# Kernel tuning notes

Measured on AMD Instinct MI355X. Metric: run time of the kernel, lower is better.

Reference implementation:

```python
import jax, jax.numpy as jnp
import numpy as np

H = 1024        # hidden_size
I = 512         # moe_intermediate_size
E = 16          # n_routed_experts
K = 2           # num_experts_per_tok
N_SHARED = 2    # n_shared_experts
IS = I * N_SHARED  # shared expert intermediate
B, S = 2, 2048


def setup_inputs() -> dict:
    key = jax.random.key(0)
    ks = jax.random.split(key, 9)
    sc = 0.02
    return {
        "hidden_states": jax.random.normal(ks[0], (B, S, H), jnp.float32),
        "router_w":     jax.random.normal(ks[1], (E, H), jnp.float32) * sc,
        "expert_gate":  jax.random.normal(ks[2], (E, H, I), jnp.float32) * sc,
        "expert_up":    jax.random.normal(ks[3], (E, H, I), jnp.float32) * sc,
        "expert_down":  jax.random.normal(ks[4], (E, I, H), jnp.float32) * sc,
        "shared_gate":  jax.random.normal(ks[5], (H, IS), jnp.float32) * sc,
        "shared_up":    jax.random.normal(ks[6], (H, IS), jnp.float32) * sc,
        "shared_down":  jax.random.normal(ks[7], (IS, H), jnp.float32) * sc,
    }


def reference(hidden_states, router_w, expert_gate, expert_up, expert_down,
              shared_gate, shared_up, shared_down):
    orig_shape = hidden_states.shape
    x = hidden_states.reshape(-1, H)            # [T, H]
    T = x.shape[0]

    # --- MoEGate: softmax router scores, top-k, normalized weights ---
    scores = jax.nn.softmax(x @ router_w.T, axis=-1)        # [T, E]
    topk_w, topk_idx = jax.lax.top_k(scores, K)             # [T, K]
    topk_w = topk_w / jnp.sum(topk_w, axis=-1, keepdims=True)  # norm_topk_prob

    # Sparse combine weights as dense [T, E] gate matrix (scatter of top-k).
    gates = jnp.zeros((T, E), x.dtype).at[jnp.arange(T)[:, None], topk_idx].add(topk_w)

    # --- Routed experts: gated SiLU MLP per expert, weighted combine ---
    g = jnp.einsum('th,ehi->tei', x, expert_gate)           # [T, E, I]
    u = jnp.einsum('th,ehi->tei', x, expert_up)             # [T, E, I]
    a = jax.nn.silu(g) * u                                  # [T, E, I]
    y = jnp.einsum('tei,eih,te->th', a, expert_down, gates) # [T, H]

    # --- Shared experts ---
    s = (jax.nn.silu(x @ shared_gate) * (x @ shared_up)) @ shared_down  # [T, H]

    return (y + s).reshape(orig_shape)
```

## Files before the change

kernel.cpp:

```cpp
#include <hip/hip_runtime.h>
#include <math.h>

#define H_DIM 1024
#define I_DIM 512
#define E_NUM 16
#define T_TOK 4096
#define IS_DIM 1024
#define CSTR 32

#define P_RT   1024
#define P_WU   (P_RT + 2048)
#define P_SG   (P_WU + 2048)
#define P_SU   (P_SG + 256)
#define P_END  (P_SU + 256)

#define G_GEMM 1152
#define G_TR   2304
#define G_END  (G_GEMM + G_TR)

#define D_GRID 896

typedef unsigned short u16;
typedef __attribute__((ext_vector_type(8))) short short8;
typedef __attribute__((ext_vector_type(4))) float floatx4;

__device__ __forceinline__ float bf2f(u16 u) {
    union { unsigned int u; float f; } c; c.u = ((unsigned int)u) << 16; return c.f;
}
__device__ __forceinline__ u16 f2bf(float f) {
    union { float f; unsigned int u; } c; c.f = f;
    unsigned int r = (c.u + 0x7fffu + ((c.u >> 16) & 1u)) >> 16;
    return (u16)r;
}
__device__ __forceinline__ void gld16(const u16* g, u16* l) {
    __builtin_amdgcn_global_load_lds(
        (const __attribute__((address_space(1))) unsigned int*)g,
        (__attribute__((address_space(3))) unsigned int*)l, 16, 0, 0);
}

__device__ __forceinline__ void tr64(const float* src, u16* dst, int R, int C,
                                     int local, u16* tile)
{
    int tpm = (R >> 6) * (C >> 6);
    int mat = local / tpm;
    int tl_ = local - mat * tpm;
    int tcn = C >> 6;
    int tr = tl_ / tcn, tc = tl_ - tr * tcn;
    src += (size_t)mat * R * C;
    dst += (size_t)mat * R * C;
    int t = threadIdx.x;
    int r0 = t >> 2, c0 = (t & 3) << 4;
    const float* sp = src + (size_t)(tr * 64 + r0) * C + tc * 64 + c0;
    #pragma unroll
    for (int j = 0; j < 16; j += 4) {
        float4 v = *(const float4*)(sp + j);
        tile[r0 * 65 + c0 + j + 0] = f2bf(v.x);
        tile[r0 * 65 + c0 + j + 1] = f2bf(v.y);
        tile[r0 * 65 + c0 + j + 2] = f2bf(v.z);
        tile[r0 * 65 + c0 + j + 3] = f2bf(v.w);
    }
    __syncthreads();
    int cW = t >> 2, rW = (t & 3) << 4;
    u16 tmp[16];
    #pragma unroll
    for (int j = 0; j < 16; ++j) tmp[j] = tile[(rW + j) * 65 + cW];
    u16* dp = dst + (size_t)(tc * 64 + cW) * R + tr * 64 + rW;
    *(uint4*)(dp)     = *(const uint4*)(tmp);
    *(uint4*)(dp + 8) = *(const uint4*)(tmp + 8);
}

__device__ __forceinline__ int derive_routed(int gi, const int* cnt,
                                             int& e, int& mt, int& sub, int& abase)
{
    int off = 0, b = 0;
    #pragma unroll
    for (int ee = 0; ee < E_NUM; ++ee) {
        int mts = (cnt[ee * CSTR] + 127) >> 7;
        int span = mts << 3;
        if (gi < off + span) {
            int local = gi - off;
            e = ee; mt = local >> 3; sub = local & 7; abase = b;
            return 1;
        }
        off += span; b += mts << 7;
    }
    return 0;
}

__global__ __launch_bounds__(256, 4)
void k_prep(const float* x, const float* rw,
            const float* wg, const float* wu, const float* sg, const float* su,
            u16* wgt, u16* wut, u16* sgt, u16* sut,
            u16* xb, float* topkw, int* elist, int* cnt)
{
    __shared__ u16 tile[64 * 65];
    int bi = blockIdx.x;
    if (bi >= P_RT) {
        if (bi < P_WU)      tr64(wg, wgt, 1024, 512,  bi - P_RT, tile);
        else if (bi < P_SG) tr64(wu, wut, 1024, 512,  bi - P_WU, tile);
        else if (bi < P_SU) tr64(sg, sgt, 1024, 1024, bi - P_SG, tile);
        else                tr64(su, sut, 1024, 1024, bi - P_SU, tile);
        return;
    }
    int lane = threadIdx.x & 63;
    int wv = threadIdx.x >> 6;
    int t = bi * 4 + wv;
    const float* xr = x + (size_t)t * H_DIM;
    float xv[16];
    #pragma unroll
    for (int j = 0; j < 16; ++j) xv[j] = xr[j * 64 + lane];
    u16* xrow = xb + (size_t)t * H_DIM;
    #pragma unroll
    for (int j = 0; j < 16; ++j) xrow[j * 64 + lane] = f2bf(xv[j]);
    float sc[E_NUM];
    #pragma unroll
    for (int e = 0; e < E_NUM; ++e) sc[e] = 0.f;
    #pragma unroll
    for (int e = 0; e < E_NUM; ++e) {
        const float* rr = rw + e * H_DIM;
        #pragma unroll
        for (int j = 0; j < 16; ++j) sc[e] += xv[j] * rr[j * 64 + lane];
    }
    #pragma unroll
    for (int off = 32; off > 0; off >>= 1) {
        float tmp[E_NUM];
        #pragma unroll
        for (int e = 0; e < E_NUM; ++e) tmp[e] = __shfl_xor(sc[e], off, 64);
        #pragma unroll
        for (int e = 0; e < E_NUM; ++e) sc[e] += tmp[e];
    }
    if (lane == 0) {
        float b1 = -1e30f, b2 = -1e30f; int i1 = 0, i2 = 0;
        #pragma unroll
        for (int e = 0; e < E_NUM; ++e) {
            if (sc[e] > b1) { b2 = b1; i2 = i1; b1 = sc[e]; i1 = e; }
            else if (sc[e] > b2) { b2 = sc[e]; i2 = e; }
        }
        float w1 = 1.f / (1.f + __expf(b2 - b1));
        float w2 = 1.f - w1;
        topkw[t * 2]     = w1;
        topkw[t * 2 + 1] = w2;
        int p1 = atomicAdd(&cnt[i1 * CSTR], 1); elist[i1 * T_TOK + p1] = (t << 1);
        int p2 = atomicAdd(&cnt[i2 * CSTR], 1); elist[i2 * T_TOK + p2] = (t << 1) | 1;
    }
}

__global__ __launch_bounds__(256, 3)
void k_gateup(const u16* xb, const u16* wgt, const u16* wut,
              const u16* sgt, const u16* sut,
              const float* wd, const float* sd, u16* wdt, u16* sdt,
              const int* elist, const int* cnt,
              u16* act, u16* sact)
{
    __shared__ u16 smem[128 * 64 + 64 * 64 + 64 * 64];
    int bi = blockIdx.x;
    if (bi >= G_GEMM) {
        int tb = bi - G_GEMM;
        if (tb < 2048) tr64(wd, wdt, 512, 1024, tb, smem);
        else           tr64(sd, sdt, 1024, 1024, tb - 2048, smem);
        return;
    }
    int kind, e = 0, mt, cb, abase = 0;
    if (bi < 512) { kind = 1; mt = bi >> 4; cb = bi & 15; }
    else {
        kind = 0;
        if (!derive_routed(bi - 512, cnt, e, mt, cb, abase)) return;
    }

    u16* lA = smem;
    u16* lG = smem + 8192;
    u16* lU = smem + 12288;
    int tid = threadIdx.x, lane = tid & 63, w = tid >> 6;
    int srow = lane >> 2, scp = lane & 3;

    const u16* gb = kind ? sgt : (wgt + (size_t)e * I_DIM * H_DIM);
    const u16* ub = kind ? sut : (wut + (size_t)e * I_DIM * H_DIM);
    int c = cnt[e * CSTR];

    const u16 *gA[2], *gG, *gU;
    u16 *dA[2], *dG, *dU;
    #pragma unroll
    for (int jj = 0; jj < 2; ++jj) {
        int call = w * 2 + jj;
        int row = call * 16 + srow;
        int gc = scp ^ ((row >> 1) & 3);
        int tok;
        if (kind) tok = mt * 128 + row;
        else {
            int p = mt * 128 + row;
            int pc = p < c ? p : c - 1;
            tok = elist[e * T_TOK + pc] >> 1;
        }
        gA[jj] = xb + (size_t)tok * H_DIM + gc * 8;
        dA[jj] = lA + call * 512;
    }
    {
        int row = w * 16 + srow;
        int gc = scp ^ ((row >> 1) & 3);
        gG = gb + (size_t)(cb * 64 + row) * H_DIM + gc * 8;
        gU = ub + (size_t)(cb * 64 + row) * H_DIM + gc * 8;
        dG = lG + w * 512;
        dU = lU + w * 512;
    }

    int wr = w >> 1, wc = w & 1;
    int quad = lane >> 4, l15 = lane & 15;
    const u16 *fA[4], *fG[2], *fU[2];
    #pragma unroll
    for (int i = 0; i < 4; ++i) {
        int r = wr * 64 + i * 16 + l15;
        fA[i] = lA + r * 32 + (quad ^ ((r >> 1) & 3)) * 8;
    }
    #pragma unroll
    for (int j = 0; j < 2; ++j) {
        int n = wc * 32 + j * 16 + l15;
        fG[j] = lG + n * 32 + (quad ^ ((n >> 1) & 3)) * 8;
        fU[j] = lU + n * 32 + (quad ^ ((n >> 1) & 3)) * 8;
    }

    floatx4 accg[4][2], accu[4][2];
    #pragma unroll
    for (int i = 0; i < 4; ++i)
        #pragma unroll
        for (int j = 0; j < 2; ++j)
            #pragma unroll
            for (int r = 0; r < 4; ++r) { accg[i][j][r] = 0.f; accu[i][j][r] = 0.f; }

    for (int s = 0; s < H_DIM / 64; ++s) {
        #pragma unroll
        for (int q = 0; q < 2; ++q) {
            gld16(gA[0] + q * 32, dA[0] + q * 4096);
            gld16(gA[1] + q * 32, dA[1] + q * 4096);
            gld16(gG + q * 32, dG + q * 2048);
            gld16(gU + q * 32, dU + q * 2048);
        }
        gA[0] += 64; gA[1] += 64; gG += 64; gU += 64;
        __syncthreads();
        #pragma unroll
        for (int q = 0; q < 2; ++q) {
            short8 a[4], g[2], u[2];
            #pragma unroll
            for (int i = 0; i < 4; ++i) a[i] = *(const short8*)(fA[i] + q * 4096);
            #pragma unroll
            for (int j = 0; j < 2; ++j) {
                g[j] = *(const short8*)(fG[j] + q * 2048);
                u[j] = *(const short8*)(fU[j] + q * 2048);
            }
            #pragma unroll
            for (int i = 0; i < 4; ++i)
                #pragma unroll
                for (int j = 0; j < 2; ++j) {
                    accg[i][j] = __builtin_amdgcn_mfma_f32_16x16x32_bf16(a[i], g[j], accg[i][j], 0, 0, 0);
                    accu[i][j] = __builtin_amdgcn_mfma_f32_16x16x32_bf16(a[i], u[j], accu[i][j], 0, 0, 0);
                }
        }
        __syncthreads();
    }

    u16* obase = kind ? (sact + (size_t)(mt * 128) * IS_DIM)
                      : (act + (size_t)(abase + mt * 128) * I_DIM);
    int old = kind ? IS_DIM : I_DIM;
    #pragma unroll
    for (int i = 0; i < 4; ++i)
        #pragma unroll
        for (int j = 0; j < 2; ++j)
            #pragma unroll
            for (int r = 0; r < 4; ++r) {
                int row = wr * 64 + i * 16 + quad * 4 + r;
                int col = cb * 64 + wc * 32 + j * 16 + l15;
                float gg = accg[i][j][r], uu = accu[i][j][r];
                float aa = gg / (1.f + __expf(-gg)) * uu;
                obase[(size_t)row * old + col] = f2bf(aa);
            }
}

__global__ __launch_bounds__(256, 3)
void k_down(const u16* act, const u16* sact, const u16* wdt, const u16* sdt,
            const int* elist, const int* cnt, const float* topkw,
            u16* y0, u16* y1, float* out)
{
    int bi = blockIdx.x;
    int kind, e = 0, mt, nb, abase = 0;
    if (bi < 256) { kind = 1; mt = bi >> 3; nb = bi & 7; }
    else {
        kind = 0;
        if (!derive_routed(bi - 256, cnt, e, mt, nb, abase)) return;
    }

    __shared__ u16 smem[128 * 64 * 2];
    u16* lA = smem;
    u16* lB = smem + 8192;
    int tid = threadIdx.x, lane = tid & 63, w = tid >> 6;
    int srow = lane >> 2, scp = lane & 3;

    int K = kind ? IS_DIM : I_DIM;
    const u16* ab = kind ? (sact + (size_t)(mt * 128) * IS_DIM)
                         : (act + (size_t)(abase + mt * 128) * I_DIM);
    const u16* bb = kind ? (sdt + (size_t)(nb * 128) * IS_DIM)
                         : (wdt + ((size_t)e * H_DIM + nb * 128) * I_DIM);
    int c = cnt[e * CSTR];

    const u16 *gA[2], *gB[2];
    u16 *dA[2], *dB[2];
    #pragma unroll
    for (int jj = 0; jj < 2; ++jj) {
        int call = w * 2 + jj;
        int row = call * 16 + srow;
        int gc = scp ^ ((row >> 1) & 3);
        gA[jj] = ab + (size_t)row * K + gc * 8;
        dA[jj] = lA + call * 512;
        gB[jj] = bb + (size_t)row * K + gc * 8;
        dB[jj] = lB + call * 512;
    }

    int wr = w >> 1, wc = w & 1;
    int quad = lane >> 4, l15 = lane & 15;
    const u16 *fA[4], *fB[4];
    #pragma unroll
    for (int i = 0; i < 4; ++i) {
        int r = wr * 64 + i * 16 + l15;
        fA[i] = lA + r * 32 + (quad ^ ((r >> 1) & 3)) * 8;
    }
    #pragma unroll
    for (int j = 0; j < 4; ++j) {
        int n = wc * 64 + j * 16 + l15;
        fB[j] = lB + n * 32 + (quad ^ ((n >> 1) & 3)) * 8;
    }

    floatx4 acc[4][4];
    #pragma unroll
    for (int i = 0; i < 4; ++i)
        #pragma unroll
        for (int j = 0; j < 4; ++j)
            #pragma unroll
            for (int r = 0; r < 4; ++r) acc[i][j][r] = 0.f;

    int steps = K >> 6;
    for (int s = 0; s < steps; ++s) {
        #pragma unroll
        for (int q = 0; q < 2; ++q) {
            gld16(gA[0] + q * 32, dA[0] + q * 4096);
            gld16(gA[1] + q * 32, dA[1] + q * 4096);
            gld16(gB[0] + q * 32, dB[0] + q * 4096);
            gld16(gB[1] + q * 32, dB[1] + q * 4096);
        }
        gA[0] += 64; gA[1] += 64; gB[0] += 64; gB[1] += 64;
        __syncthreads();
        #pragma unroll
        for (int q = 0; q < 2; ++q) {
            short8 a[4], b[4];
            #pragma unroll
            for (int i = 0; i < 4; ++i) a[i] = *(const short8*)(fA[i] + q * 4096);
            #pragma unroll
            for (int j = 0; j < 4; ++j) b[j] = *(const short8*)(fB[j] + q * 4096);
            #pragma unroll
            for (int i = 0; i < 4; ++i)
                #pragma unroll
                for (int j = 0; j < 4; ++j)
                    acc[i][j] = __builtin_amdgcn_mfma_f32_16x16x32_bf16(a[i], b[j], acc[i][j], 0, 0, 0);
        }
        __syncthreads();
    }

    if (kind) {
        #pragma unroll
        for (int i = 0; i < 4; ++i)
            #pragma unroll
            for (int j = 0; j < 4; ++j)
                #pragma unroll
                for (int r = 0; r < 4; ++r) {
                    int row = mt * 128 + wr * 64 + i * 16 + quad * 4 + r;
                    int col = nb * 128 + wc * 64 + j * 16 + l15;
                    out[(size_t)row * H_DIM + col] = acc[i][j][r];
                }
    } else {
        #pragma unroll
        for (int i = 0; i < 4; ++i)
            #pragma unroll
            for (int r = 0; r < 4; ++r) {
                int row = wr * 64 + i * 16 + quad * 4 + r;
                int p = mt * 128 + row;
                if (p < c) {
                    int ent = elist[e * T_TOK + p];
                    int t = ent >> 1, sl = ent & 1;
                    float wt = topkw[t * 2 + sl];
                    u16* yb = sl ? y1 : y0;
                    #pragma unroll
                    for (int j = 0; j < 4; ++j) {
                        int col = nb * 128 + wc * 64 + j * 16 + l15;
                        yb[(size_t)t * H_DIM + col] = f2bf(wt * acc[i][j][r]);
                    }
                }
            }
    }
}

__global__ __launch_bounds__(256)
void k_final(float* out, const u16* y0, const u16* y1)
{
    int i = blockIdx.x * 256 + threadIdx.x;
    float4 o = ((const float4*)out)[i];
    uint2 a = ((const uint2*)y0)[i];
    uint2 b = ((const uint2*)y1)[i];
    const u16* pa = (const u16*)&a;
    const u16* pb = (const u16*)&b;
    o.x += bf2f(pa[0]) + bf2f(pb[0]);
    o.y += bf2f(pa[1]) + bf2f(pb[1]);
    o.z += bf2f(pa[2]) + bf2f(pb[2]);
    o.w += bf2f(pa[3]) + bf2f(pb[3]);
    ((float4*)out)[i] = o;
}

extern "C" void kernel_launch(void* const* d_in, const int* in_sizes, int n_in,
                              void* d_out, int out_size, void* d_ws, size_t ws_size,
                              hipStream_t stream)
{
    const float* x  = (const float*)d_in[0];
    const float* rw = (const float*)d_in[1];
    const float* wg = (const float*)d_in[2];
    const float* wu = (const float*)d_in[3];
    const float* wd = (const float*)d_in[4];
    const float* sg = (const float*)d_in[5];
    const float* su = (const float*)d_in[6];
    const float* sd = (const float*)d_in[7];
    float* out = (float*)d_out;

    char* ws = (char*)d_ws;
    const size_t MB = 1024ull * 1024ull;
    u16* wgt  = (u16*)(ws);
    u16* wut  = (u16*)(ws + 16 * MB);
    u16* wdt  = (u16*)(ws + 32 * MB);
    u16* sgt  = (u16*)(ws + 48 * MB);
    u16* sut  = (u16*)(ws + 50 * MB);
    u16* sdt  = (u16*)(ws + 52 * MB);
    u16* xb   = (u16*)(ws + 54 * MB);
    u16* act  = (u16*)(ws + 62 * MB);
    u16* sact = (u16*)(ws + 72 * MB);
    u16* y0   = (u16*)(ws + 80 * MB);
    u16* y1   = (u16*)(ws + 88 * MB);
    float* topkw  = (float*)(ws + 96 * MB);
    int* elist    = (int*)(ws + 96 * MB + 64 * 1024);
    int* cnt      = (int*)(ws + 97 * MB);

    hipMemsetAsync(cnt, 0, E_NUM * CSTR * sizeof(int), stream);
    k_prep<<<P_END, 256, 0, stream>>>(x, rw, wg, wu, sg, su,
                                      wgt, wut, sgt, sut,
                                      xb, topkw, elist, cnt);
    k_gateup<<<G_END, 256, 0, stream>>>(xb, wgt, wut, sgt, sut,
                                        wd, sd, wdt, sdt,
                                        elist, cnt, act, sact);
    k_down<<<D_GRID, 256, 0, stream>>>(act, sact, wdt, sdt,
                                       elist, cnt, topkw, y0, y1, out);
    k_final<<<T_TOK * H_DIM / 4 / 256, 256, 0, stream>>>(out, y0, y1);
}
```

Baseline: 271.1 us.

## Enlarge gate/up and down GEMM tiles and add block index swizzle

Doubles the N-tile of the gate/up GEMM from 64 to 128 columns and of the down GEMM from 128 to 256 columns, halving the grid sizes and the number of routed sub-tiles per expert. Each block now reuses every loaded A tile across more weight columns, cutting redundant reads of activations and the per-block fixed overhead. Block indices are also permuted across groups of 8 to change how neighbouring blocks are scheduled. The larger accumulator arrays raise register and LDS use, and occupancy hints drop from 3 to 2 blocks per CU, which could reduce latency hiding and leave fewer blocks to fill the machine. The workspace offsets are also shifted.

```diff
diff --git a/kernel.cpp b/kernel.cpp
--- a/kernel.cpp
+++ b/kernel.cpp
@@ -14,11 +14,11 @@
 #define P_SU   (P_SG + 256)
 #define P_END  (P_SU + 256)
 
-#define G_GEMM 1152
+#define G_GEMM 576
 #define G_TR   2304
 #define G_END  (G_GEMM + G_TR)
 
-#define D_GRID 896
+#define D_GRID 448
 
 typedef unsigned short u16;
 typedef __attribute__((ext_vector_type(8))) short short8;
@@ -76,10 +76,10 @@
     #pragma unroll
     for (int ee = 0; ee < E_NUM; ++ee) {
         int mts = (cnt[ee * CSTR] + 127) >> 7;
-        int span = mts << 3;
+        int span = mts << 2;
         if (gi < off + span) {
             int local = gi - off;
-            e = ee; mt = local >> 3; sub = local & 7; abase = b;
+            e = ee; mt = local >> 2; sub = local & 3; abase = b;
             return 1;
         }
         off += span; b += mts << 7;
@@ -145,14 +145,14 @@
     }
 }
 
-__global__ __launch_bounds__(256, 3)
+__global__ __launch_bounds__(256, 2)
 void k_gateup(const u16* xb, const u16* wgt, const u16* wut,
               const u16* sgt, const u16* sut,
               const float* wd, const float* sd, u16* wdt, u16* sdt,
               const int* elist, const int* cnt,
               u16* act, u16* sact)
 {
-    __shared__ u16 smem[128 * 64 + 64 * 64 + 64 * 64];
+    __shared__ u16 smem[24576];
     int bi = blockIdx.x;
     if (bi >= G_GEMM) {
         int tb = bi - G_GEMM;
@@ -160,16 +160,14 @@
         else           tr64(sd, sdt, 1024, 1024, tb - 2048, smem);
         return;
     }
+    bi = (bi & 7) * (G_GEMM / 8) + (bi >> 3);
     int kind, e = 0, mt, cb, abase = 0;
-    if (bi < 512) { kind = 1; mt = bi >> 4; cb = bi & 15; }
+    if (bi < 256) { kind = 1; mt = bi >> 3; cb = bi & 7; }
     else {
         kind = 0;
-        if (!derive_routed(bi - 512, cnt, e, mt, cb, abase)) return;
-    }
-
-    u16* lA = smem;
-    u16* lG = smem + 8192;
-    u16* lU = smem + 12288;
+        if (!derive_routed(bi - 256, cnt, e, mt, cb, abase)) return;
+    }
+
     int tid = threadIdx.x, lane = tid & 63, w = tid >> 6;
     int srow = lane >> 2, scp = lane & 3;
 
@@ -177,12 +175,11 @@
     const u16* ub = kind ? sut : (wut + (size_t)e * I_DIM * H_DIM);
     int c = cnt[e * CSTR];
 
-    const u16 *gA[2], *gG, *gU;
-    u16 *dA[2], *dG, *dU;
-    #pragma unroll
-    for (int jj = 0; jj < 2; ++jj) {
-        int call = w * 2 + jj;
-        int row = call * 16 + srow;
+    const u16 *pA[2], *pG[2], *pU[2];
+    int dA[2], dB[2];
+    #pragma unroll
+    for (int i = 0; i < 2; ++i) {
+        int row = w * 32 + i * 16 + srow;
         int gc = scp ^ ((row >> 1) & 3);
         int tok;
         if (kind) tok = mt * 128 + row;
@@ -191,65 +188,64 @@
             int pc = p < c ? p : c - 1;
             tok = elist[e * T_TOK + pc] >> 1;
         }
-        gA[jj] = xb + (size_t)tok * H_DIM + gc * 8;
-        dA[jj] = lA + call * 512;
-    }
-    {
-        int row = w * 16 + srow;
-        int gc = scp ^ ((row >> 1) & 3);
-        gG = gb + (size_t)(cb * 64 + row) * H_DIM + gc * 8;
-        gU = ub + (size_t)(cb * 64 + row) * H_DIM + gc * 8;
-        dG = lG + w * 512;
-        dU = lU + w * 512;
+        pA[i] = xb + (size_t)tok * H_DIM + gc * 8;
+        dA[i] = w * 1024 + i * 512;
+        int n = cb * 128 + row;
+        pG[i] = gb + (size_t)n * H_DIM + gc * 8;
+        pU[i] = ub + (size_t)n * H_DIM + gc * 8;
+        dB[i] = w * 1024 + i * 512;
     }
 
     int wr = w >> 1, wc = w & 1;
     int quad = lane >> 4, l15 = lane & 15;
-    const u16 *fA[4], *fG[2], *fU[2];
+    int fA[4], fB[4];
     #pragma unroll
     for (int i = 0; i < 4; ++i) {
         int r = wr * 64 + i * 16 + l15;
-        fA[i] = lA + r * 32 + (quad ^ ((r >> 1) & 3)) * 8;
-    }
-    #pragma unroll
-    for (int j = 0; j < 2; ++j) {
-        int n = wc * 32 + j * 16 + l15;
-        fG[j] = lG + n * 32 + (quad ^ ((n >> 1) & 3)) * 8;
-        fU[j] = lU + n * 32 + (quad ^ ((n >> 1) & 3)) * 8;
-    }
-
-    floatx4 accg[4][2], accu[4][2];
+        fA[i] = r * 32 + (quad ^ ((r >> 1) & 3)) * 8;
+    }
+    #pragma unroll
+    for (int j = 0; j < 4; ++j) {
+        int n = wc * 64 + j * 16 + l15;
+        fB[j] = n * 32 + (quad ^ ((n >> 1) & 3)) * 8;
+    }
+
+    floatx4 accg[4][4], accu[4][4];
     #pragma unroll
     for (int i = 0; i < 4; ++i)
         #pragma unroll
-        for (int j = 0; j < 2; ++j)
+        for (int j = 0; j < 4; ++j)
             #pragma unroll
             for (int r = 0; r < 4; ++r) { accg[i][j][r] = 0.f; accu[i][j][r] = 0.f; }
 
     for (int s = 0; s < H_DIM / 64; ++s) {
         #pragma unroll
         for (int q = 0; q < 2; ++q) {
-            gld16(gA[0] + q * 32, dA[0] + q * 4096);
-            gld16(gA[1] + q * 32, dA[1] + q * 4096);
-            gld16(gG + q * 32, dG + q * 2048);
-            gld16(gU + q * 32, dU + q * 2048);
-        }
-        gA[0] += 64; gA[1] += 64; gG += 64; gU += 64;
+            int k = s * 64 + q * 32;
+            u16* c0 = smem + q * 4096;
+            gld16(pA[0] + k, c0 + dA[0]);
+            gld16(pA[1] + k, c0 + dA[1]);
+            gld16(pG[0] + k, c0 + 8192 + dB[0]);
+            gld16(pG[1] + k, c0 + 8192 + dB[1]);
+            gld16(pU[0] + k, c0 + 16384 + dB[0]);
+            gld16(pU[1] + k, c0 + 16384 + dB[1]);
+        }
         __syncthreads();
         #pragma unroll
         for (int q = 0; q < 2; ++q) {
-            short8 a[4], g[2], u[2];
-            #pragma unroll
-            for (int i = 0; i < 4; ++i) a[i] = *(const short8*)(fA[i] + q * 4096);
-            #pragma unroll
-            for (int j = 0; j < 2; ++j) {
-                g[j] = *(const short8*)(fG[j] + q * 2048);
-                u[j] = *(const short8*)(fU[j] + q * 2048);
+            const u16* cb_ = smem + q * 4096;
+            short8 a[4], g[4], u[4];
+            #pragma unroll
+            for (int i = 0; i < 4; ++i) a[i] = *(const short8*)(cb_ + fA[i]);
+            #pragma unroll
+            for (int j = 0; j < 4; ++j) {
+                g[j] = *(const short8*)(cb_ + 8192 + fB[j]);
+                u[j] = *(const short8*)(cb_ + 16384 + fB[j]);
             }
             #pragma unroll
             for (int i = 0; i < 4; ++i)
                 #pragma unroll
-                for (int j = 0; j < 2; ++j) {
+                for (int j = 0; j < 4; ++j) {
                     accg[i][j] = __builtin_amdgcn_mfma_f32_16x16x32_bf16(a[i], g[j], accg[i][j], 0, 0, 0);
                     accu[i][j] = __builtin_amdgcn_mfma_f32_16x16x32_bf16(a[i], u[j], accu[i][j], 0, 0, 0);
                 }
@@ -263,75 +259,78 @@
     #pragma unroll
     for (int i = 0; i < 4; ++i)
         #pragma unroll
-        for (int j = 0; j < 2; ++j)
+        for (int j = 0; j < 4; ++j)
             #pragma unroll
             for (int r = 0; r < 4; ++r) {
                 int row = wr * 64 + i * 16 + quad * 4 + r;
-                int col = cb * 64 + wc * 32 + j * 16 + l15;
+                int col = cb * 128 + wc * 64 + j * 16 + l15;
                 float gg = accg[i][j][r], uu = accu[i][j][r];
                 float aa = gg / (1.f + __expf(-gg)) * uu;
                 obase[(size_t)row * old + col] = f2bf(aa);
             }
 }
 
-__global__ __launch_bounds__(256, 3)
+__global__ __launch_bounds__(256, 2)
 void k_down(const u16* act, const u16* sact, const u16* wdt, const u16* sdt,
             const int* elist, const int* cnt, const float* topkw,
             u16* y0, u16* y1, float* out)
 {
     int bi = blockIdx.x;
+    bi = (bi & 7) * (D_GRID / 8) + (bi >> 3);
     int kind, e = 0, mt, nb, abase = 0;
-    if (bi < 256) { kind = 1; mt = bi >> 3; nb = bi & 7; }
+    if (bi < 128) { kind = 1; mt = bi >> 2; nb = bi & 3; }
     else {
         kind = 0;
-        if (!derive_routed(bi - 256, cnt, e, mt, nb, abase)) return;
-    }
-
-    __shared__ u16 smem[128 * 64 * 2];
-    u16* lA = smem;
-    u16* lB = smem + 8192;
+        if (!derive_routed(bi - 128, cnt, e, mt, nb, abase)) return;
+    }
+
+    __shared__ u16 smem[24576];
     int tid = threadIdx.x, lane = tid & 63, w = tid >> 6;
     int srow = lane >> 2, scp = lane & 3;
 
     int K = kind ? IS_DIM : I_DIM;
     const u16* ab = kind ? (sact + (size_t)(mt * 128) * IS_DIM)
                          : (act + (size_t)(abase + mt * 128) * I_DIM);
-    const u16* bb = kind ? (sdt + (size_t)(nb * 128) * IS_DIM)
-                         : (wdt + ((size_t)e * H_DIM + nb * 128) * I_DIM);
+    const u16* bb = kind ? sdt : (wdt + (size_t)e * H_DIM * I_DIM);
     int c = cnt[e * CSTR];
 
-    const u16 *gA[2], *gB[2];
-    u16 *dA[2], *dB[2];
-    #pragma unroll
-    for (int jj = 0; jj < 2; ++jj) {
-        int call = w * 2 + jj;
-        int row = call * 16 + srow;
+    const u16 *pA[2], *pB[4];
+    int dA[2], dB[4];
+    #pragma unroll
+    for (int i = 0; i < 2; ++i) {
+        int row = w * 32 + i * 16 + srow;
         int gc = scp ^ ((row >> 1) & 3);
-        gA[jj] = ab + (size_t)row * K + gc * 8;
-        dA[jj] = lA + call * 512;
-        gB[jj] = bb + (size_t)row * K + gc * 8;
-        dB[jj] = lB + call * 512;
+        pA[i] = ab + (size_t)row * K + gc * 8;
+        dA[i] = w * 1024 + i * 512;
+    }
+    #pragma unroll
+    for (int i = 0; i < 4; ++i) {
+        int ln = w * 64 + i * 16 + srow;
+        int n = nb * 256 + ln;
+        int gc = scp ^ ((ln >> 1) & 3);
+        pB[i] = bb + (size_t)n * K + gc * 8;
+        dB[i] = w * 2048 + i * 512;
     }
 
     int wr = w >> 1, wc = w & 1;
     int quad = lane >> 4, l15 = lane & 15;
-    const u16 *fA[4], *fB[4];
+    int fA[4], fB[8];
     #pragma unroll
     for (int i = 0; i < 4; ++i) {
         int r = wr * 64 + i * 16 + l15;
-        fA[i] = lA + r * 32 + (quad ^ ((r >> 1) & 3)) * 8;
-    }
-    #pragma unroll
-    for (int j = 0; j < 4; ++j) {
-        int n = wc * 64 + j * 16 + l15;
-        fB[j] = lB + n * 32 + (quad ^ ((n >> 1) & 3)) * 8;
-    }
-
-    floatx4 acc[4][4];
+        fA[i] = r * 32 + (quad ^ ((r >> 1) & 3)) * 8;
+    }
+    #pragma unroll
+    for (int j = 0; j < 8; ++j) {
+        int n = wc * 128 + j * 16 + l15;
+        fB[j] = n * 32 + (quad ^ ((n >> 1) & 3)) * 8;
+    }
+
+    floatx4 acc[4][8];
     #pragma unroll
     for (int i = 0; i < 4; ++i)
         #pragma unroll
-        for (int j = 0; j < 4; ++j)
+        for (int j = 0; j < 8; ++j)
             #pragma unroll
             for (int r = 0; r < 4; ++r) acc[i][j][r] = 0.f;
 
@@ -339,24 +338,28 @@
     for (int s = 0; s < steps; ++s) {
         #pragma unroll
         for (int q = 0; q < 2; ++q) {
-            gld16(gA[0] + q * 32, dA[0] + q * 4096);
-            gld16(gA[1] + q * 32, dA[1] + q * 4096);
-            gld16(gB[0] + q * 32, dB[0] + q * 4096);
-            gld16(gB[1] + q * 32, dB[1] + q * 4096);
-        }
-        gA[0] += 64; gA[1] += 64; gB[0] += 64; gB[1] += 64;
+            int k = s * 64 + q * 32;
+            u16* cA = smem + q * 4096;
+            u16* cB = smem + 8192 + q * 8192;
+            gld16(pA[0] + k, cA + dA[0]);
+            gld16(pA[1] + k, cA + dA[1]);
+            #pragma unroll
+            for (int i = 0; i < 4; ++i) gld16(pB[i] + k, cB + dB[i]);
+        }
         __syncthreads();
         #pragma unroll
         for (int q = 0; q < 2; ++q) {
-            short8 a[4], b[4];
-            #pragma unroll
-            for (int i = 0; i < 4; ++i) a[i] = *(const short8*)(fA[i] + q * 4096);
-            #pragma unroll
-            for (int j = 0; j < 4; ++j) b[j] = *(const short8*)(fB[j] + q * 4096);
+            const u16* cA = smem + q * 4096;
+            const u16* cB = smem + 8192 + q * 8192;
+            short8 a[4], b[8];
+            #pragma unroll
+            for (int i = 0; i < 4; ++i) a[i] = *(const short8*)(cA + fA[i]);
+            #pragma unroll
+            for (int j = 0; j < 8; ++j) b[j] = *(const short8*)(cB + fB[j]);
             #pragma unroll
             for (int i = 0; i < 4; ++i)
                 #pragma unroll
-                for (int j = 0; j < 4; ++j)
+                for (int j = 0; j < 8; ++j)
                     acc[i][j] = __builtin_amdgcn_mfma_f32_16x16x32_bf16(a[i], b[j], acc[i][j], 0, 0, 0);
         }
         __syncthreads();
@@ -366,13 +369,14 @@
         #pragma unroll
         for (int i = 0; i < 4; ++i)
             #pragma unroll
-            for (int j = 0; j < 4; ++j)
+            for (int r = 0; r < 4; ++r) {
+                int row = mt * 128 + wr * 64 + i * 16 + quad * 4 + r;
                 #pragma unroll
-                for (int r = 0; r < 4; ++r) {
-                    int row = mt * 128 + wr * 64 + i * 16 + quad * 4 + r;
-                    int col = nb * 128 + wc * 64 + j * 16 + l15;
+                for (int j = 0; j < 8; ++j) {
+                    int col = nb * 256 + wc * 128 + j * 16 + l15;
                     out[(size_t)row * H_DIM + col] = acc[i][j][r];
                 }
+            }
     } else {
         #pragma unroll
         for (int i = 0; i < 4; ++i)
@@ -386,8 +390,8 @@
                     float wt = topkw[t * 2 + sl];
                     u16* yb = sl ? y1 : y0;
                     #pragma unroll
-                    for (int j = 0; j < 4; ++j) {
-                        int col = nb * 128 + wc * 64 + j * 16 + l15;
+                    for (int j = 0; j < 8; ++j) {
+                        int col = nb * 256 + wc * 128 + j * 16 + l15;
                         yb[(size_t)t * H_DIM + col] = f2bf(wt * acc[i][j][r]);
                     }
                 }
@@ -435,12 +439,12 @@
     u16* sdt  = (u16*)(ws + 52 * MB);
     u16* xb   = (u16*)(ws + 54 * MB);
     u16* act  = (u16*)(ws + 62 * MB);
-    u16* sact = (u16*)(ws + 72 * MB);
-    u16* y0   = (u16*)(ws + 80 * MB);
-    u16* y1   = (u16*)(ws + 88 * MB);
-    float* topkw  = (float*)(ws + 96 * MB);
-    int* elist    = (int*)(ws + 96 * MB + 64 * 1024);
-    int* cnt      = (int*)(ws + 97 * MB);
+    u16* sact = (u16*)(ws + 74 * MB);
+    u16* y0   = (u16*)(ws + 82 * MB);
+    u16* y1   = (u16*)(ws + 90 * MB);
+    float* topkw  = (float*)(ws + 98 * MB);
+    int* elist    = (int*)(ws + 98 * MB + 64 * 1024);
+    int* cnt      = (int*)(ws + 99 * MB);
 
     hipMemsetAsync(cnt, 0, E_NUM * CSTR * sizeof(int), stream);
     k_prep<<<P_END, 256, 0, stream>>>(x, rw, wg, wu, sg, su,
```

Result: slower. 280.2 us (+3.3%).

## Split down-projection into routed and shared kernels, fuse final combine into shared epilogue

Applied to the files above, without the earlier changes.

Splits the combined down-projection kernel into a routed-expert kernel and a shared-expert kernel launched after it. The shared kernel's epilogue reads the routed bf16 partials y0/y1 and writes the final sum directly, which removes the separate k_final pass and one read/write of the fp32 output. The cost is that the shared GEMM no longer overlaps with the routed blocks in a single grid, so there is a serialization point between the two launches. The epilogue also does scattered bf16 loads per element.

```diff
diff --git a/kernel.cpp b/kernel.cpp
--- a/kernel.cpp
+++ b/kernel.cpp
@@ -18,7 +18,8 @@
 #define G_TR   2304
 #define G_END  (G_GEMM + G_TR)
 
-#define D_GRID 896
+#define DR_GRID 640
+#define DS_GRID 256
 
 typedef unsigned short u16;
 typedef __attribute__((ext_vector_type(8))) short short8;
@@ -275,17 +276,12 @@
 }
 
 __global__ __launch_bounds__(256, 3)
-void k_down(const u16* act, const u16* sact, const u16* wdt, const u16* sdt,
-            const int* elist, const int* cnt, const float* topkw,
-            u16* y0, u16* y1, float* out)
-{
-    int bi = blockIdx.x;
-    int kind, e = 0, mt, nb, abase = 0;
-    if (bi < 256) { kind = 1; mt = bi >> 3; nb = bi & 7; }
-    else {
-        kind = 0;
-        if (!derive_routed(bi - 256, cnt, e, mt, nb, abase)) return;
-    }
+void k_down_r(const u16* act, const u16* wdt,
+              const int* elist, const int* cnt, const float* topkw,
+              u16* y0, u16* y1)
+{
+    int e = 0, mt, nb, abase = 0;
+    if (!derive_routed(blockIdx.x, cnt, e, mt, nb, abase)) return;
 
     __shared__ u16 smem[128 * 64 * 2];
     u16* lA = smem;
@@ -293,11 +289,8 @@
     int tid = threadIdx.x, lane = tid & 63, w = tid >> 6;
     int srow = lane >> 2, scp = lane & 3;
 
-    int K = kind ? IS_DIM : I_DIM;
-    const u16* ab = kind ? (sact + (size_t)(mt * 128) * IS_DIM)
-                         : (act + (size_t)(abase + mt * 128) * I_DIM);
-    const u16* bb = kind ? (sdt + (size_t)(nb * 128) * IS_DIM)
-                         : (wdt + ((size_t)e * H_DIM + nb * 128) * I_DIM);
+    const u16* ab = act + (size_t)(abase + mt * 128) * I_DIM;
+    const u16* bb = wdt + ((size_t)e * H_DIM + nb * 128) * I_DIM;
     int c = cnt[e * CSTR];
 
     const u16 *gA[2], *gB[2];
@@ -307,9 +300,9 @@
         int call = w * 2 + jj;
         int row = call * 16 + srow;
         int gc = scp ^ ((row >> 1) & 3);
-        gA[jj] = ab + (size_t)row * K + gc * 8;
+        gA[jj] = ab + (size_t)row * I_DIM + gc * 8;
         dA[jj] = lA + call * 512;
-        gB[jj] = bb + (size_t)row * K + gc * 8;
+        gB[jj] = bb + (size_t)row * I_DIM + gc * 8;
         dB[jj] = lB + call * 512;
     }
 
@@ -335,8 +328,7 @@
             #pragma unroll
             for (int r = 0; r < 4; ++r) acc[i][j][r] = 0.f;
 
-    int steps = K >> 6;
-    for (int s = 0; s < steps; ++s) {
+    for (int s = 0; s < I_DIM / 64; ++s) {
         #pragma unroll
         for (int q = 0; q < 2; ++q) {
             gld16(gA[0] + q * 32, dA[0] + q * 4096);
@@ -362,53 +354,115 @@
         __syncthreads();
     }
 
-    if (kind) {
-        #pragma unroll
-        for (int i = 0; i < 4; ++i)
-            #pragma unroll
-            for (int j = 0; j < 4; ++j)
+    #pragma unroll
+    for (int i = 0; i < 4; ++i)
+        #pragma unroll
+        for (int r = 0; r < 4; ++r) {
+            int row = wr * 64 + i * 16 + quad * 4 + r;
+            int p = mt * 128 + row;
+            if (p < c) {
+                int ent = elist[e * T_TOK + p];
+                int t = ent >> 1, sl = ent & 1;
+                float wt = topkw[t * 2 + sl];
+                u16* yb = sl ? y1 : y0;
                 #pragma unroll
-                for (int r = 0; r < 4; ++r) {
-                    int row = mt * 128 + wr * 64 + i * 16 + quad * 4 + r;
+                for (int j = 0; j < 4; ++j) {
                     int col = nb * 128 + wc * 64 + j * 16 + l15;
-                    out[(size_t)row * H_DIM + col] = acc[i][j][r];
-                }
-    } else {
-        #pragma unroll
-        for (int i = 0; i < 4; ++i)
-            #pragma unroll
-            for (int r = 0; r < 4; ++r) {
-                int row = wr * 64 + i * 16 + quad * 4 + r;
-                int p = mt * 128 + row;
-                if (p < c) {
-                    int ent = elist[e * T_TOK + p];
-                    int t = ent >> 1, sl = ent & 1;
-                    float wt = topkw[t * 2 + sl];
-                    u16* yb = sl ? y1 : y0;
-                    #pragma unroll
-                    for (int j = 0; j < 4; ++j) {
-                        int col = nb * 128 + wc * 64 + j * 16 + l15;
-                        yb[(size_t)t * H_DIM + col] = f2bf(wt * acc[i][j][r]);
-                    }
+                    yb[(size_t)t * H_DIM + col] = f2bf(wt * acc[i][j][r]);
                 }
             }
-    }
-}
-
-__global__ __launch_bounds__(256)
-void k_final(float* out, const u16* y0, const u16* y1)
-{
-    int i = blockIdx.x * 256 + threadIdx.x;
-    float4 o = ((const float4*)out)[i];
-    uint2 a = ((const uint2*)y0)[i];
-    uint2 b = ((const uint2*)y1)[i];
-    const u16* pa = (const u16*)&a;
-    const u16* pb = (const u16*)&b;
-    o.x += bf2f(pa[0]) + bf2f(pb[0]);
-    o.y += bf2f(pa[1]) + bf2f(pb[1]);
-    o.z += bf2f(pa[2]) + bf2f(pb[2]);
-    o.w += bf2f(pa[3]) + bf2f(pb[3]);
-    ((float4*)out)[i] = o;
+        }
+}
+
+__global__ __launch_bounds__(256, 3)
+void k_down_s(const u16* sact, const u16* sdt, const u16* y0, const u16* y1,
+              float* out)
+{
+    int bi = blockIdx.x;
+    int mt = bi >> 3, nb = bi & 7;
+
+    __shared__ u16 smem[128 * 64 * 2];
+    u16* lA = smem;
+    u16* lB = smem + 8192;
+    int tid = threadIdx.x, lane = tid & 63, w = tid >> 6;
+    int srow = lane >> 2, scp = lane & 3;
+
+    const u16* ab = sact + (size_t)(mt * 128) * IS_DIM;
+    const u16* bb = sdt + (size_t)(nb * 128) * IS_DIM;
+
+    const u16 *gA[2], *gB[2];
+    u16 *dA[2], *dB[2];
+    #pragma unroll
+    for (int jj = 0; jj < 2; ++jj) {
+        int call = w * 2 + jj;
+        int row = call * 16 + srow;
+        int gc = scp ^ ((row >> 1) & 3);
+        gA[jj] = ab + (size_t)row * IS_DIM + gc * 8;
+        dA[jj] = lA + call * 512;
+        gB[jj] = bb + (size_t)row * IS_DIM + gc * 8;
+        dB[jj] = lB + call * 512;
+    }
+
+    int wr = w >> 1, wc = w & 1;
+    int quad = lane >> 4, l15 = lane & 15;
+    const u16 *fA[4], *fB[4];
+    #pragma unroll
+    for (int i = 0; i < 4; ++i) {
+        int r = wr * 64 + i * 16 + l15;
+        fA[i] = lA + r * 32 + (quad ^ ((r >> 1) & 3)) * 8;
+    }
+    #pragma unroll
+    for (int j = 0; j < 4; ++j) {
+        int n = wc * 64 + j * 16 + l15;
+        fB[j] = lB + n * 32 + (quad ^ ((n >> 1) & 3)) * 8;
+    }
+
+    floatx4 acc[4][4];
+    #pragma unroll
+    for (int i = 0; i < 4; ++i)
+        #pragma unroll
+        for (int j = 0; j < 4; ++j)
+            #pragma unroll
+            for (int r = 0; r < 4; ++r) acc[i][j][r] = 0.f;
+
+    for (int s = 0; s < IS_DIM / 64; ++s) {
+        #pragma unroll
+        for (int q = 0; q < 2; ++q) {
+            gld16(gA[0] + q * 32, dA[0] + q * 4096);
+            gld16(gA[1] + q * 32, dA[1] + q * 4096);
+            gld16(gB[0] + q * 32, dB[0] + q * 4096);
+            gld16(gB[1] + q * 32, dB[1] + q * 4096);
+        }
+        gA[0] += 64; gA[1] += 64; gB[0] += 64; gB[1] += 64;
+        __syncthreads();
+        #pragma unroll
+        for (int q = 0; q < 2; ++q) {
+            short8 a[4], b[4];
+            #pragma unroll
+            for (int i = 0; i < 4; ++i) a[i] = *(const short8*)(fA[i] + q * 4096);
+            #pragma unroll
+            for (int j = 0; j < 4; ++j) b[j] = *(const short8*)(fB[j] + q * 4096);
+            #pragma unroll
+            for (int i = 0; i < 4; ++i)
+                #pragma unroll
+                for (int j = 0; j < 4; ++j)
+                    acc[i][j] = __builtin_amdgcn_mfma_f32_16x16x32_bf16(a[i], b[j], acc[i][j], 0, 0, 0);
+        }
+        __syncthreads();
+    }
+
+    #pragma unroll
+    for (int i = 0; i < 4; ++i)
+        #pragma unroll
+        for (int r = 0; r < 4; ++r) {
+            int row = mt * 128 + wr * 64 + i * 16 + quad * 4 + r;
+            #pragma unroll
+            for (int j = 0; j < 4; ++j) {
+                int col = nb * 128 + wc * 64 + j * 16 + l15;
+                size_t idx = (size_t)row * H_DIM + col;
+                out[idx] = acc[i][j][r] + bf2f(y0[idx]) + bf2f(y1[idx]);
+            }
+        }
 }
 
 extern "C" void kernel_launch(void* const* d_in, const int* in_sizes, int n_in,
@@ -449,7 +503,6 @@
     k_gateup<<<G_END, 256, 0, stream>>>(xb, wgt, wut, sgt, sut,
                                         wd, sd, wdt, sdt,
                                         elist, cnt, act, sact);
-    k_down<<<D_GRID, 256, 0, stream>>>(act, sact, wdt, sdt,
-                                       elist, cnt, topkw, y0, y1, out);
-    k_final<<<T_TOK * H_DIM / 4 / 256, 256, 0, stream>>>(out, y0, y1);
-}
+    k_down_r<<<DR_GRID, 256, 0, stream>>>(act, wdt, elist, cnt, topkw, y0, y1);
+    k_down_s<<<DS_GRID, 256, 0, stream>>>(sact, sdt, y0, y1, out);
+}
```

Result: slower. 277.5 us (+2.3%).
